# Performance work log

Hardware: AMD Instinct MI355X
Metric: run time of the kernel (lower is better)

## Reference

```python
import jax, jax.numpy as jnp
import numpy as np

EMBED_DIM = 1024
HEADS = 16
HEAD_DIM = EMBED_DIM // HEADS
DIST_LAMBDA = -0.1
LN_EPS = 1e-5


def setup_inputs() -> dict:
    key = jax.random.key(0)
    ks = jax.random.split(key, 16)
    B, N, D = 32, 4096, EMBED_DIM
    s = 1.0 / np.sqrt(D)
    inp = {
        "query": jax.random.normal(ks[0], (B, D), jnp.float32),
        "context": jax.random.normal(ks[1], (B, N, D), jnp.float32),
        "dist_matrix": jax.random.uniform(ks[2], (B, 1, N), jnp.float32),
        "context_mask": jax.random.randint(ks[3], (B, N), 0, 2, jnp.int32),
        "Wq": jax.random.normal(ks[4], (D, D), jnp.float32) * s,
        "bq": jnp.zeros((D,), jnp.float32),
        "Wk": jax.random.normal(ks[5], (D, D), jnp.float32) * s,
        "bk": jnp.zeros((D,), jnp.float32),
        "Wv": jax.random.normal(ks[6], (D, D), jnp.float32) * s,
        "bv": jnp.zeros((D,), jnp.float32),
        "Wo": jax.random.normal(ks[7], (D, D), jnp.float32) * s,
        "bo": jnp.zeros((D,), jnp.float32),
        "ln_gamma": jnp.ones((D,), jnp.float32),
        "ln_beta": jnp.zeros((D,), jnp.float32),
    }
    return inp


def reference(query, context, dist_matrix, context_mask,
              Wq, bq, Wk, bk, Wv, bv, Wo, bo, ln_gamma, ln_beta):
    B, N, D = context.shape
    H, hd = HEADS, HEAD_DIM
    # projections
    q = (query @ Wq + bq).reshape(B, H, hd)            # [B,H,hd] (single query)
    k = (context @ Wk + bk).reshape(B, N, H, hd)       # [B,N,H,hd]
    v = (context @ Wv + bv).reshape(B, N, H, hd)
    # scores: [B,H,N]
    scores = jnp.einsum("bhd,bnhd->bhn", q, k) / np.sqrt(hd)
    # additive Manhattan-distance bias, broadcast over heads
    scores = scores + dist_matrix * DIST_LAMBDA        # dist_matrix [B,1,N]
    # mask
    scores = jnp.where(context_mask[:, None, :] == 0, -1e9, scores)
    attn = jax.nn.softmax(scores, axis=-1)             # [B,H,N]
    attn_out = jnp.einsum("bhn,bnhd->bhd", attn, v).reshape(B, D)
    output = attn_out @ Wo + bo
    x = query + output
    # LayerNorm
    mu = jnp.mean(x, axis=-1, keepdims=True)
    var = jnp.mean((x - mu) ** 2, axis=-1, keepdims=True)
    return (x - mu) * jax.lax.rsqrt(var + LN_EPS) * ln_gamma + ln_beta
```

## Files before the change

### kernel.cpp

```cpp
#include <hip/hip_runtime.h>
#include <hip/hip_bf16.h>
#include <math.h>

#define DDIM 1024
#define NH 16
#define HDIM 64
#define SCALE 0.125f
#define DLAM -0.1f
#define LNEPS 1e-5f
#define NS 16
#define CHW 16
#define BROW 256
#define CBSTR 1032

typedef short bf16x8 __attribute__((ext_vector_type(8)));
typedef float f32x4 __attribute__((ext_vector_type(4)));

__device__ inline unsigned short f2bf(float x) {
    return __builtin_bit_cast(unsigned short, __float2bfloat16(x));
}
__device__ inline float bfhi2f(unsigned u) {
    return __builtin_bit_cast(float, u & 0xffff0000u);
}
__device__ inline float bflo2f(unsigned u) {
    return __builtin_bit_cast(float, u << 16);
}

__global__ __launch_bounds__(512) void k_q(const float* __restrict__ query,
                                           const float* __restrict__ Wq,
                                           const float* __restrict__ bq,
                                           float* __restrict__ qout) {
    int b = blockIdx.x, c0 = blockIdx.y * 128;
    __shared__ float qs[DDIM];
    __shared__ float ps[512];
    int t = threadIdx.x;
    for (int i = t; i < DDIM; i += 512) qs[i] = query[b * DDIM + i];
    __syncthreads();
    int cl = t & 127;
    int col = c0 + cl;
    int d0 = (t >> 7) * 256;
    float acc = 0.f;
#pragma unroll 8
    for (int d = d0; d < d0 + 256; ++d)
        acc = fmaf(qs[d], Wq[(size_t)d * DDIM + col], acc);
    ps[t] = acc;
    __syncthreads();
    if (t < 128)
        qout[b * DDIM + col] = ps[t] + ps[t + 128] + ps[t + 256] + ps[t + 384] + bq[col];
}

__global__ __launch_bounds__(256) void k_qp(const float* __restrict__ qin,
                                            const float* __restrict__ Wk,
                                            unsigned short* __restrict__ qpb) {
    int dt = blockIdx.x, bg = blockIdx.y;
    __shared__ float qs[8][DDIM];
    for (int i = threadIdx.x; i < 8 * DDIM; i += 256)
        qs[i >> 10][i & 1023] =
            qin[(size_t)(bg * 8 + (i >> 10)) * DDIM + (i & 1023)];
    __syncthreads();
    int h = threadIdx.x & 15, dl = threadIdx.x >> 4;
    int d = dt * 16 + dl;
    const float* wr = Wk + (size_t)d * DDIM + h * HDIM;
    float acc[8] = {0.f, 0.f, 0.f, 0.f, 0.f, 0.f, 0.f, 0.f};
#pragma unroll
    for (int j = 0; j < HDIM; ++j) {
        float wv = wr[j];
#pragma unroll
        for (int bb = 0; bb < 8; ++bb)
            acc[bb] = fmaf(wv, qs[bb][h * HDIM + j], acc[bb]);
    }
#pragma unroll
    for (int bb = 0; bb < 8; ++bb)
        qpb[((size_t)((bg * 8 + bb) * NH + h)) * DDIM + d] = f2bf(acc[bb] * SCALE);
}

__global__ __launch_bounds__(512) void k_sb(const float* __restrict__ qin,
                                            const float* __restrict__ bk,
                                            float* __restrict__ sb) {
    int idx = threadIdx.x;
    int b = idx >> 4, h = idx & 15;
    float acc = 0.f;
#pragma unroll
    for (int j = 0; j < HDIM; ++j)
        acc = fmaf(bk[h * HDIM + j], qin[b * DDIM + h * HDIM + j], acc);
    sb[idx] = acc * SCALE;
}

__global__ __launch_bounds__(256, 2) void k_flash2(
    const float* __restrict__ ctx, const unsigned short* __restrict__ qpb,
    const float* __restrict__ sb, const float* __restrict__ dist,
    const int* __restrict__ mask, float* __restrict__ partA,
    float* __restrict__ partM, float* __restrict__ partL, int N) {
    __shared__ unsigned short cbuf[2][CHW][CBSTR];
    __shared__ float red[4][CHW][17];
    __shared__ float P_lds[CHW][20];
    __shared__ float fh_lds[NH];
    __shared__ float dls[BROW];

    int b = blockIdx.x, ns = blockIdx.y;
    int t = threadIdx.x, lane = t & 63, w = t >> 6;
    int m = lane & 15, g = lane >> 4;
    int nb0 = ns * BROW;
    const int NIT = BROW / CHW;

    {
        float dv = dist[(size_t)b * N + nb0 + t] * DLAM;
        dls[t] = mask[(size_t)b * N + nb0 + t] ? dv : -1e30f;
    }
    bf16x8 qf[8];
#pragma unroll
    for (int j = 0; j < 8; ++j)
        qf[j] = *reinterpret_cast<const bf16x8*>(
            qpb + ((size_t)(b * NH + m)) * DDIM + w * 256 + j * 32 + g * 8);
    float sbv = sb[b * NH + m];

    f32x4 acc[NH];
#pragma unroll
    for (int h = 0; h < NH; ++h) acc[h] = (f32x4){0.f, 0.f, 0.f, 0.f};
    float m_run = -1e30f, l_run = 0.f;

    const float4* cb4 = reinterpret_cast<const float4*>(ctx) +
                        ((size_t)b * N + nb0) * (DDIM / 4);
    float4 inflight[16];

#define LOADC(c)                                                  \
    {                                                             \
        const float4* src = cb4 + (size_t)(c) * CHW * (DDIM / 4); \
        _Pragma("unroll") for (int i = 0; i < 16; ++i)            \
            inflight[i] = src[i * 256 + t];                       \
    }
#define WRITECB(buf)                                                         \
    {                                                                        \
        _Pragma("unroll") for (int i = 0; i < 16; ++i) {                     \
            float4 v = inflight[i];                                          \
            unsigned lo = (unsigned)f2bf(v.x) | ((unsigned)f2bf(v.y) << 16); \
            unsigned hi = (unsigned)f2bf(v.z) | ((unsigned)f2bf(v.w) << 16); \
            *reinterpret_cast<uint2*>(&cbuf[buf][i][t * 4]) =                \
                make_uint2(lo, hi);                                          \
        }                                                                    \
    }

    LOADC(0);
    WRITECB(0);
    LOADC(1);

    int dq = w * 256 + lane * 4;
    for (int c = 0; c < NIT; ++c) {
        __syncthreads();
        int buf = c & 1;
        if (c + 1 < NIT) {
            WRITECB(buf ^ 1);
            if (c + 2 < NIT) LOADC(c + 2);
        }
        f32x4 cS = {0.f, 0.f, 0.f, 0.f};
#pragma unroll
        for (int j = 0; j < 8; ++j) {
            bf16x8 a = *reinterpret_cast<const bf16x8*>(
                &cbuf[buf][m][w * 256 + j * 32 + g * 8]);
            cS = __builtin_amdgcn_mfma_f32_16x16x32_bf16(a, qf[j], cS, 0, 0, 0);
        }
#pragma unroll
        for (int r = 0; r < 4; ++r) red[w][g * 4 + r][m] = cS[r];
        __syncthreads();
        float S[4];
#pragma unroll
        for (int r = 0; r < 4; ++r) {
            int n = g * 4 + r;
            S[r] = red[0][n][m] + red[1][n][m] + red[2][n][m] + red[3][n][m] +
                   sbv + dls[c * CHW + n];
        }
        float cm = fmaxf(fmaxf(S[0], S[1]), fmaxf(S[2], S[3]));
        cm = fmaxf(cm, __shfl_xor(cm, 16, 64));
        cm = fmaxf(cm, __shfl_xor(cm, 32, 64));
        float mnew = fmaxf(m_run, cm);
        float f = __expf(m_run - mnew);
        float p[4];
        float ls = 0.f;
#pragma unroll
        for (int r = 0; r < 4; ++r) {
            p[r] = __expf(S[r] - mnew);
            ls += p[r];
        }
        ls += __shfl_xor(ls, 16, 64);
        ls += __shfl_xor(ls, 32, 64);
        l_run = l_run * f + ls;
        m_run = mnew;
#pragma unroll
        for (int r = 0; r < 4; ++r) P_lds[g * 4 + r][m] = p[r];
        if (w == 0 && g == 0) fh_lds[m] = f;
        __syncthreads();
#pragma unroll
        for (int h = 0; h < NH; ++h) acc[h] *= fh_lds[h];
#pragma unroll 4
        for (int n = 0; n < CHW; ++n) {
            uint2 cw = *reinterpret_cast<const uint2*>(&cbuf[buf][n][dq]);
            float cv0 = bflo2f(cw.x), cv1 = bfhi2f(cw.x);
            float cv2 = bflo2f(cw.y), cv3 = bfhi2f(cw.y);
            float4 P0 = *reinterpret_cast<const float4*>(&P_lds[n][0]);
            float4 P1 = *reinterpret_cast<const float4*>(&P_lds[n][4]);
            float4 P2 = *reinterpret_cast<const float4*>(&P_lds[n][8]);
            float4 P3 = *reinterpret_cast<const float4*>(&P_lds[n][12]);
            float Pv[16] = {P0.x, P0.y, P0.z, P0.w, P1.x, P1.y, P1.z, P1.w,
                            P2.x, P2.y, P2.z, P2.w, P3.x, P3.y, P3.z, P3.w};
#pragma unroll
            for (int h = 0; h < NH; ++h) {
                acc[h][0] = fmaf(Pv[h], cv0, acc[h][0]);
                acc[h][1] = fmaf(Pv[h], cv1, acc[h][1]);
                acc[h][2] = fmaf(Pv[h], cv2, acc[h][2]);
                acc[h][3] = fmaf(Pv[h], cv3, acc[h][3]);
            }
        }
    }

#pragma unroll
    for (int h = 0; h < NH; ++h) {
        float4 o = make_float4(acc[h][0], acc[h][1], acc[h][2], acc[h][3]);
        *reinterpret_cast<float4*>(
            partA + ((size_t)((b * NS + ns) * NH + h)) * DDIM + dq) = o;
    }
    if (t < NH) {
        partM[(b * NS + ns) * NH + t] = m_run;
        partL[(b * NS + ns) * NH + t] = l_run;
    }
#undef LOADC
#undef WRITECB
}

__global__ __launch_bounds__(256) void k_comb(const float* __restrict__ partA,
                                              const float* __restrict__ partM,
                                              const float* __restrict__ partL,
                                              float* __restrict__ ctxa) {
    int row = blockIdx.x;
    int b = row >> 4, h = row & 15;
    float M = -1e30f;
#pragma unroll
    for (int ns = 0; ns < NS; ++ns)
        M = fmaxf(M, partM[(b * NS + ns) * NH + h]);
    float denom = 0.f;
#pragma unroll
    for (int ns = 0; ns < NS; ++ns)
        denom = fmaf(__expf(partM[(b * NS + ns) * NH + h] - M),
                     partL[(b * NS + ns) * NH + h], denom);
    float inv = 1.f / denom;
    int d4 = threadIdx.x * 4;
    float4 a = make_float4(0.f, 0.f, 0.f, 0.f);
#pragma unroll 8
    for (int ns = 0; ns < NS; ++ns) {
        float wv = __expf(partM[(b * NS + ns) * NH + h] - M);
        float4 v = *reinterpret_cast<const float4*>(
            partA + ((size_t)((b * NS + ns) * NH + h)) * DDIM + d4);
        a.x = fmaf(wv, v.x, a.x);
        a.y = fmaf(wv, v.y, a.y);
        a.z = fmaf(wv, v.z, a.z);
        a.w = fmaf(wv, v.w, a.w);
    }
    float4 o = make_float4(a.x * inv, a.y * inv, a.z * inv, a.w * inv);
    *reinterpret_cast<float4*>(ctxa + (size_t)row * DDIM + d4) = o;
}

__global__ __launch_bounds__(256) void k_vproj(const float* __restrict__ ctxa,
                                               const float* __restrict__ Wv,
                                               const float* __restrict__ bv,
                                               float* __restrict__ oattn) {
    int b = blockIdx.x, c0 = blockIdx.y * 128;
    int h0 = c0 >> 6;
    __shared__ float cs[2][DDIM];
    __shared__ float ps[256];
    for (int i = threadIdx.x; i < 2 * DDIM; i += 256)
        cs[i >> 10][i & 1023] =
            ctxa[((size_t)(b * NH + h0 + (i >> 10))) * DDIM + (i & 1023)];
    __syncthreads();
    int t = threadIdx.x;
    int cl = t & 127;
    int col = c0 + cl;
    int hl = cl >> 6;
    int d0 = (t >> 7) * 512;
    float acc = 0.f;
#pragma unroll 8
    for (int d = d0; d < d0 + 512; ++d)
        acc = fmaf(cs[hl][d], Wv[(size_t)d * DDIM + col], acc);
    ps[t] = acc;
    __syncthreads();
    if (t < 128) oattn[b * DDIM + col] = ps[t] + ps[t + 128] + bv[col];
}

__global__ __launch_bounds__(256) void k_oproj(const float* __restrict__ query,
                                               const float* __restrict__ oattn,
                                               const float* __restrict__ Wo,
                                               const float* __restrict__ bo,
                                               float* __restrict__ x) {
    int b = blockIdx.x, c0 = blockIdx.y * 128;
    __shared__ float os[DDIM];
    __shared__ float ps[256];
    for (int i = threadIdx.x; i < DDIM; i += 256) os[i] = oattn[b * DDIM + i];
    __syncthreads();
    int t = threadIdx.x;
    int col = c0 + (t & 127);
    int d0 = (t >> 7) * 512;
    float acc = 0.f;
#pragma unroll 8
    for (int d = d0; d < d0 + 512; ++d)
        acc = fmaf(os[d], Wo[(size_t)d * DDIM + col], acc);
    ps[t] = acc;
    __syncthreads();
    if (t < 128)
        x[b * DDIM + col] = query[b * DDIM + col] + ps[t] + ps[t + 128] + bo[col];
}

__global__ __launch_bounds__(256) void k_ln(const float* __restrict__ x,
                                            const float* __restrict__ gamma,
                                            const float* __restrict__ beta,
                                            float* __restrict__ out) {
    int b = blockIdx.x;
    int t = threadIdx.x;
    __shared__ float red[8];
    float xv[4];
    float lsum = 0.f;
#pragma unroll
    for (int k = 0; k < 4; ++k) {
        xv[k] = x[b * DDIM + t + k * 256];
        lsum += xv[k];
    }
#pragma unroll
    for (int off = 32; off > 0; off >>= 1) lsum += __shfl_xor(lsum, off, 64);
    if ((t & 63) == 0) red[t >> 6] = lsum;
    __syncthreads();
    float mu = (red[0] + red[1] + red[2] + red[3]) * (1.f / DDIM);
    float lsq = 0.f;
#pragma unroll
    for (int k = 0; k < 4; ++k) {
        float dx = xv[k] - mu;
        lsq += dx * dx;
    }
#pragma unroll
    for (int off = 32; off > 0; off >>= 1) lsq += __shfl_xor(lsq, off, 64);
    if ((t & 63) == 0) red[4 + (t >> 6)] = lsq;
    __syncthreads();
    float var = (red[4] + red[5] + red[6] + red[7]) * (1.f / DDIM);
    float rstd = rsqrtf(var + LNEPS);
#pragma unroll
    for (int k = 0; k < 4; ++k) {
        int c = t + k * 256;
        out[b * DDIM + c] = (xv[k] - mu) * rstd * gamma[c] + beta[c];
    }
}

extern "C" void kernel_launch(void* const* d_in, const int* in_sizes, int n_in,
                              void* d_out, int out_size, void* d_ws, size_t ws_size,
                              hipStream_t stream) {
    const float* query = (const float*)d_in[0];
    const float* ctx   = (const float*)d_in[1];
    const float* dist  = (const float*)d_in[2];
    const int*   mask  = (const int*)d_in[3];
    const float* Wq = (const float*)d_in[4];
    const float* bq = (const float*)d_in[5];
    const float* Wk = (const float*)d_in[6];
    const float* bk = (const float*)d_in[7];
    const float* Wv = (const float*)d_in[8];
    const float* bv = (const float*)d_in[9];
    const float* Wo = (const float*)d_in[10];
    const float* bo = (const float*)d_in[11];
    const float* gamma = (const float*)d_in[12];
    const float* beta  = (const float*)d_in[13];
    float* out = (float*)d_out;

    int B = in_sizes[0] / DDIM;
    int N = in_sizes[1] / (B * DDIM);

    float* ws = (float*)d_ws;
    float* q = ws;
    unsigned short* qpb = (unsigned short*)(q + (size_t)B * DDIM);
    float* sb = (float*)(qpb + (size_t)B * NH * DDIM);
    float* partA = sb + (size_t)B * NH;
    float* partM = partA + (size_t)B * NS * NH * DDIM;
    float* partL = partM + (size_t)B * NS * NH;
    float* ctxa = partL + (size_t)B * NS * NH;
    float* oattn = ctxa + (size_t)B * NH * DDIM;
    float* xbuf = oattn + (size_t)B * DDIM;

    k_q<<<dim3(B, 8), 512, 0, stream>>>(query, Wq, bq, q);
    k_qp<<<dim3(DDIM / 16, B / 8), 256, 0, stream>>>(q, Wk, qpb);
    k_sb<<<1, B * NH, 0, stream>>>(q, bk, sb);
    k_flash2<<<dim3(B, NS), 256, 0, stream>>>(ctx, qpb, sb, dist, mask,
                                              partA, partM, partL, N);
    k_comb<<<B * NH, 256, 0, stream>>>(partA, partM, partL, ctxa);
    k_vproj<<<dim3(B, 8), 256, 0, stream>>>(ctxa, Wv, bv, oattn);
    k_oproj<<<dim3(B, 8), 256, 0, stream>>>(query, oattn, Wo, bo, xbuf);
    k_ln<<<B, 256, 0, stream>>>(xbuf, gamma, beta, out);
}
```

Measured before the change: 242.8 us.

## Batch 8 rows per block in small GEMVs and fuse split combine into V projection

The Q, V and O projection kernels now each process 8 batch rows per block, so every weight element loaded from global memory is reused across 8 accumulators instead of one. This cuts weight traffic for Wq, Wv and Wo by roughly 8x. The split-softmax combine kernel is merged into the V projection, removing the ctxa intermediate buffer and one launch. In exchange, far fewer blocks are launched (32-64 per kernel), which lowers parallelism, and shared memory per block grows to about 40KB.

```diff
diff --git a/kernel.cpp b/kernel.cpp
--- a/kernel.cpp
+++ b/kernel.cpp
@@ -26,27 +26,35 @@
     return __builtin_bit_cast(float, u << 16);
 }
 
-__global__ __launch_bounds__(512) void k_q(const float* __restrict__ query,
-                                           const float* __restrict__ Wq,
-                                           const float* __restrict__ bq,
-                                           float* __restrict__ qout) {
-    int b = blockIdx.x, c0 = blockIdx.y * 128;
-    __shared__ float qs[DDIM];
-    __shared__ float ps[512];
+__global__ __launch_bounds__(256) void k_qb(const float* __restrict__ query,
+                                            const float* __restrict__ Wq,
+                                            const float* __restrict__ bq,
+                                            float* __restrict__ qout) {
+    int c0 = blockIdx.x * 128, bg = blockIdx.y;
+    __shared__ float qs[8][DDIM];
+    __shared__ float ps[2][8][128];
     int t = threadIdx.x;
-    for (int i = t; i < DDIM; i += 512) qs[i] = query[b * DDIM + i];
-    __syncthreads();
-    int cl = t & 127;
+    for (int i = t; i < 8 * DDIM; i += 256)
+        qs[i >> 10][i & 1023] = query[(size_t)(bg * 8 + (i >> 10)) * DDIM + (i & 1023)];
+    __syncthreads();
+    int cl = t & 127, dh = t >> 7;
     int col = c0 + cl;
-    int d0 = (t >> 7) * 256;
-    float acc = 0.f;
-#pragma unroll 8
-    for (int d = d0; d < d0 + 256; ++d)
-        acc = fmaf(qs[d], Wq[(size_t)d * DDIM + col], acc);
-    ps[t] = acc;
-    __syncthreads();
-    if (t < 128)
-        qout[b * DDIM + col] = ps[t] + ps[t + 128] + ps[t + 256] + ps[t + 384] + bq[col];
+    float acc[8] = {0.f, 0.f, 0.f, 0.f, 0.f, 0.f, 0.f, 0.f};
+#pragma unroll 4
+    for (int d = dh * 512; d < dh * 512 + 512; ++d) {
+        float wv = Wq[(size_t)d * DDIM + col];
+#pragma unroll
+        for (int bb = 0; bb < 8; ++bb) acc[bb] = fmaf(qs[bb][d], wv, acc[bb]);
+    }
+#pragma unroll
+    for (int bb = 0; bb < 8; ++bb) ps[dh][bb][cl] = acc[bb];
+    __syncthreads();
+    if (dh == 0) {
+#pragma unroll
+        for (int bb = 0; bb < 8; ++bb)
+            qout[(size_t)(bg * 8 + bb) * DDIM + col] =
+                ps[0][bb][cl] + ps[1][bb][cl] + bq[col];
+    }
 }
 
 __global__ __launch_bounds__(256) void k_qp(const float* __restrict__ qin,
@@ -226,85 +234,99 @@
 #undef WRITECB
 }
 
-__global__ __launch_bounds__(256) void k_comb(const float* __restrict__ partA,
-                                              const float* __restrict__ partM,
-                                              const float* __restrict__ partL,
-                                              float* __restrict__ ctxa) {
-    int row = blockIdx.x;
-    int b = row >> 4, h = row & 15;
-    float M = -1e30f;
-#pragma unroll
-    for (int ns = 0; ns < NS; ++ns)
-        M = fmaxf(M, partM[(b * NS + ns) * NH + h]);
-    float denom = 0.f;
-#pragma unroll
-    for (int ns = 0; ns < NS; ++ns)
-        denom = fmaf(__expf(partM[(b * NS + ns) * NH + h] - M),
-                     partL[(b * NS + ns) * NH + h], denom);
-    float inv = 1.f / denom;
-    int d4 = threadIdx.x * 4;
-    float4 a = make_float4(0.f, 0.f, 0.f, 0.f);
-#pragma unroll 8
-    for (int ns = 0; ns < NS; ++ns) {
-        float wv = __expf(partM[(b * NS + ns) * NH + h] - M);
-        float4 v = *reinterpret_cast<const float4*>(
-            partA + ((size_t)((b * NS + ns) * NH + h)) * DDIM + d4);
-        a.x = fmaf(wv, v.x, a.x);
-        a.y = fmaf(wv, v.y, a.y);
-        a.z = fmaf(wv, v.z, a.z);
-        a.w = fmaf(wv, v.w, a.w);
-    }
-    float4 o = make_float4(a.x * inv, a.y * inv, a.z * inv, a.w * inv);
-    *reinterpret_cast<float4*>(ctxa + (size_t)row * DDIM + d4) = o;
-}
-
-__global__ __launch_bounds__(256) void k_vproj(const float* __restrict__ ctxa,
+__global__ __launch_bounds__(256) void k_combv(const float* __restrict__ partA,
+                                               const float* __restrict__ partM,
+                                               const float* __restrict__ partL,
                                                const float* __restrict__ Wv,
                                                const float* __restrict__ bv,
                                                float* __restrict__ oattn) {
-    int b = blockIdx.x, c0 = blockIdx.y * 128;
-    int h0 = c0 >> 6;
-    __shared__ float cs[2][DDIM];
-    __shared__ float ps[256];
-    for (int i = threadIdx.x; i < 2 * DDIM; i += 256)
-        cs[i >> 10][i & 1023] =
-            ctxa[((size_t)(b * NH + h0 + (i >> 10))) * DDIM + (i & 1023)];
-    __syncthreads();
+    int h = blockIdx.x, bg = blockIdx.y;
+    __shared__ float cs[8][DDIM];
+    __shared__ float wn_s[8][NS];
+    __shared__ float ps[4][8][64];
     int t = threadIdx.x;
-    int cl = t & 127;
+    if (t < 8) {
+        int b = bg * 8 + t;
+        float M = -1e30f;
+#pragma unroll
+        for (int ns = 0; ns < NS; ++ns)
+            M = fmaxf(M, partM[(b * NS + ns) * NH + h]);
+        float den = 0.f;
+#pragma unroll
+        for (int ns = 0; ns < NS; ++ns)
+            den = fmaf(__expf(partM[(b * NS + ns) * NH + h] - M),
+                       partL[(b * NS + ns) * NH + h], den);
+        float inv = 1.f / den;
+#pragma unroll
+        for (int ns = 0; ns < NS; ++ns)
+            wn_s[t][ns] = __expf(partM[(b * NS + ns) * NH + h] - M) * inv;
+    }
+    __syncthreads();
+    for (int i = t; i < 8 * DDIM; i += 256) {
+        int bb = i >> 10, d = i & 1023;
+        int b = bg * 8 + bb;
+        float s = 0.f;
+#pragma unroll
+        for (int ns = 0; ns < NS; ++ns)
+            s = fmaf(wn_s[bb][ns],
+                     partA[((size_t)((b * NS + ns) * NH + h)) * DDIM + d], s);
+        cs[bb][d] = s;
+    }
+    __syncthreads();
+    int cl = t & 63, qd = t >> 6;
+    int col = h * HDIM + cl;
+    float acc[8] = {0.f, 0.f, 0.f, 0.f, 0.f, 0.f, 0.f, 0.f};
+#pragma unroll 4
+    for (int d = qd * 256; d < qd * 256 + 256; ++d) {
+        float wv = Wv[(size_t)d * DDIM + col];
+#pragma unroll
+        for (int bb = 0; bb < 8; ++bb) acc[bb] = fmaf(cs[bb][d], wv, acc[bb]);
+    }
+#pragma unroll
+    for (int bb = 0; bb < 8; ++bb) ps[qd][bb][cl] = acc[bb];
+    __syncthreads();
+    if (qd == 0) {
+#pragma unroll
+        for (int bb = 0; bb < 8; ++bb)
+            oattn[(size_t)(bg * 8 + bb) * DDIM + col] =
+                ps[0][bb][cl] + ps[1][bb][cl] + ps[2][bb][cl] + ps[3][bb][cl] +
+                bv[col];
+    }
+}
+
+__global__ __launch_bounds__(256) void k_oprojb(const float* __restrict__ query,
+                                                const float* __restrict__ oattn,
+                                                const float* __restrict__ Wo,
+                                                const float* __restrict__ bo,
+                                                float* __restrict__ x) {
+    int c0 = blockIdx.x * 128, bg = blockIdx.y;
+    __shared__ float os[8][DDIM];
+    __shared__ float ps[2][8][128];
+    int t = threadIdx.x;
+    for (int i = t; i < 8 * DDIM; i += 256)
+        os[i >> 10][i & 1023] =
+            oattn[(size_t)(bg * 8 + (i >> 10)) * DDIM + (i & 1023)];
+    __syncthreads();
+    int cl = t & 127, dh = t >> 7;
     int col = c0 + cl;
-    int hl = cl >> 6;
-    int d0 = (t >> 7) * 512;
-    float acc = 0.f;
-#pragma unroll 8
-    for (int d = d0; d < d0 + 512; ++d)
-        acc = fmaf(cs[hl][d], Wv[(size_t)d * DDIM + col], acc);
-    ps[t] = acc;
-    __syncthreads();
-    if (t < 128) oattn[b * DDIM + col] = ps[t] + ps[t + 128] + bv[col];
-}
-
-__global__ __launch_bounds__(256) void k_oproj(const float* __restrict__ query,
-                                               const float* __restrict__ oattn,
-                                               const float* __restrict__ Wo,
-                                               const float* __restrict__ bo,
-                                               float* __restrict__ x) {
-    int b = blockIdx.x, c0 = blockIdx.y * 128;
-    __shared__ float os[DDIM];
-    __shared__ float ps[256];
-    for (int i = threadIdx.x; i < DDIM; i += 256) os[i] = oattn[b * DDIM + i];
-    __syncthreads();
-    int t = threadIdx.x;
-    int col = c0 + (t & 127);
-    int d0 = (t >> 7) * 512;
-    float acc = 0.f;
-#pragma unroll 8
-    for (int d = d0; d < d0 + 512; ++d)
-        acc = fmaf(os[d], Wo[(size_t)d * DDIM + col], acc);
-    ps[t] = acc;
-    __syncthreads();
-    if (t < 128)
-        x[b * DDIM + col] = query[b * DDIM + col] + ps[t] + ps[t + 128] + bo[col];
+    float acc[8] = {0.f, 0.f, 0.f, 0.f, 0.f, 0.f, 0.f, 0.f};
+#pragma unroll 4
+    for (int d = dh * 512; d < dh * 512 + 512; ++d) {
+        float wv = Wo[(size_t)d * DDIM + col];
+#pragma unroll
+        for (int bb = 0; bb < 8; ++bb) acc[bb] = fmaf(os[bb][d], wv, acc[bb]);
+    }
+#pragma unroll
+    for (int bb = 0; bb < 8; ++bb) ps[dh][bb][cl] = acc[bb];
+    __syncthreads();
+    if (dh == 0) {
+#pragma unroll
+        for (int bb = 0; bb < 8; ++bb) {
+            int b = bg * 8 + bb;
+            x[(size_t)b * DDIM + col] = query[(size_t)b * DDIM + col] +
+                                        ps[0][bb][cl] + ps[1][bb][cl] + bo[col];
+        }
+    }
 }
 
 __global__ __launch_bounds__(256) void k_ln(const float* __restrict__ x,
@@ -374,17 +396,15 @@
     float* partA = sb + (size_t)B * NH;
     float* partM = partA + (size_t)B * NS * NH * DDIM;
     float* partL = partM + (size_t)B * NS * NH;
-    float* ctxa = partL + (size_t)B * NS * NH;
-    float* oattn = ctxa + (size_t)B * NH * DDIM;
+    float* oattn = partL + (size_t)B * NS * NH;
     float* xbuf = oattn + (size_t)B * DDIM;
 
-    k_q<<<dim3(B, 8), 512, 0, stream>>>(query, Wq, bq, q);
+    k_qb<<<dim3(8, B / 8), 256, 0, stream>>>(query, Wq, bq, q);
     k_qp<<<dim3(DDIM / 16, B / 8), 256, 0, stream>>>(q, Wk, qpb);
     k_sb<<<1, B * NH, 0, stream>>>(q, bk, sb);
     k_flash2<<<dim3(B, NS), 256, 0, stream>>>(ctx, qpb, sb, dist, mask,
                                               partA, partM, partL, N);
-    k_comb<<<B * NH, 256, 0, stream>>>(partA, partM, partL, ctxa);
-    k_vproj<<<dim3(B, 8), 256, 0, stream>>>(ctxa, Wv, bv, oattn);
-    k_oproj<<<dim3(B, 8), 256, 0, stream>>>(query, oattn, Wo, bo, xbuf);
+    k_combv<<<dim3(NH, B / 8), 256, 0, stream>>>(partA, partM, partL, Wv, bv, oattn);
+    k_oprojb<<<dim3(8, B / 8), 256, 0, stream>>>(query, oattn, Wo, bo, xbuf);
     k_ln<<<B, 256, 0, stream>>>(xbuf, gamma, beta, out);
 }
```

Result: slower. 325.7 us (+34.1%).
